# Kernel optimization log

Measured on AMD Instinct MI355X. Metric: run time of the kernel, lower is better.

## Reference

```python
import jax, jax.numpy as jnp
import numpy as np

B, IN, H = 4096, 1024, 1024


def setup_inputs() -> dict:
    key = jax.random.key(0)
    ks = jax.random.split(key, 16)
    s = 1.0 / np.sqrt(IN)
    inp = {
        "x_t": jax.random.normal(ks[0], (B, IN), jnp.float32),
        "h_prev": jax.random.normal(ks[1], (B, H), jnp.float32),
        "c_prev": jax.random.normal(ks[2], (B, H), jnp.float32),
        "W_xi": jax.random.uniform(ks[3], (H, IN), jnp.float32, -s, s),
        "W_hi": jax.random.normal(ks[4], (H, H), jnp.float32) / np.sqrt(H),
        "b_i": jnp.zeros((H,), jnp.float32),
        "W_xf": jax.random.uniform(ks[5], (H, IN), jnp.float32, -s, s),
        "W_hf": jax.random.normal(ks[6], (H, H), jnp.float32) / np.sqrt(H),
        "b_f": jnp.ones((H,), jnp.float32),
        "W_xg": jax.random.uniform(ks[7], (H, IN), jnp.float32, -s, s),
        "W_hg": jax.random.normal(ks[8], (H, H), jnp.float32) / np.sqrt(H),
        "b_g": jnp.zeros((H,), jnp.float32),
        "W_xo": jax.random.uniform(ks[9], (H, IN), jnp.float32, -s, s),
        "W_ho": jax.random.normal(ks[10], (H, H), jnp.float32) / np.sqrt(H),
        "b_o": jnp.zeros((H,), jnp.float32),
    }
    return inp


def reference(x_t, h_prev, c_prev,
              W_xi, W_hi, b_i,
              W_xf, W_hf, b_f,
              W_xg, W_hg, b_g,
              W_xo, W_ho, b_o):
    # i/f/g/o gates: sigmoid/sigmoid/tanh/sigmoid of (x W_x^T + h W_h^T + b)
    i_t = jax.nn.sigmoid(x_t @ W_xi.T + h_prev @ W_hi.T + b_i)
    f_t = jax.nn.sigmoid(x_t @ W_xf.T + h_prev @ W_hf.T + b_f)
    g_t = jnp.tanh(x_t @ W_xg.T + h_prev @ W_hg.T + b_g)
    o_t = jax.nn.sigmoid(x_t @ W_xo.T + h_prev @ W_ho.T + b_o)
    c_t = f_t * c_prev + i_t * g_t
    h_t = o_t * jnp.tanh(c_t)
    return (h_t, c_t)
```

## Files before the change

### kernel.cpp

```cpp
#include <hip/hip_runtime.h>
#include <hip/hip_bf16.h>


constexpr int Mdim = 4096;
constexpr int Ndim = 4096;
constexpr int Kdim = 2048;
constexpr int Hdim = 1024;
constexpr int BM = 256;
constexpr int BN = 256;
constexpr int BK = 32;
constexpr int NT = Kdim / BK;

using short8 = __attribute__((ext_vector_type(8))) short;
using f32x4  = __attribute__((ext_vector_type(4))) float;

__device__ __forceinline__ float sigmoid_(float x) {
    return 1.f / (1.f + __expf(-x));
}
__device__ __forceinline__ float tanh_(float x) {
    float e = __expf(2.f * x);
    return (e - 1.f) / (e + 1.f);
}

__global__ void build_A(const float* __restrict__ x, const float* __restrict__ h,
                        __hip_bfloat16* __restrict__ A) {
    int idx = blockIdx.x * 256 + threadIdx.x;
    int row = idx >> 8;
    int c8  = (idx & 255) * 8;
    const float* src = (c8 < 1024) ? (x + (size_t)row * 1024 + c8)
                                   : (h + (size_t)row * 1024 + (c8 - 1024));
    float4 f0 = ((const float4*)src)[0];
    float4 f1 = ((const float4*)src)[1];
    union { short8 v; __hip_bfloat16 e[8]; } u;
    u.e[0] = __float2bfloat16(f0.x); u.e[1] = __float2bfloat16(f0.y);
    u.e[2] = __float2bfloat16(f0.z); u.e[3] = __float2bfloat16(f0.w);
    u.e[4] = __float2bfloat16(f1.x); u.e[5] = __float2bfloat16(f1.y);
    u.e[6] = __float2bfloat16(f1.z); u.e[7] = __float2bfloat16(f1.w);
    *(short8*)(A + (size_t)row * Kdim + c8) = u.v;
}

__global__ void build_B(const float* __restrict__ Wxi, const float* __restrict__ Whi,
                        const float* __restrict__ Wxf, const float* __restrict__ Whf,
                        const float* __restrict__ Wxg, const float* __restrict__ Whg,
                        const float* __restrict__ Wxo, const float* __restrict__ Who,
                        __hip_bfloat16* __restrict__ B) {
    int idx = blockIdx.x * 256 + threadIdx.x;
    int n  = idx >> 8;
    int c8 = (idx & 255) * 8;
    int g = (n >> 4) & 3;
    int j = ((n >> 6) << 4) | (n & 15);
    const float* Wx = (g == 0) ? Wxi : (g == 1) ? Wxf : (g == 2) ? Wxg : Wxo;
    const float* Wh = (g == 0) ? Whi : (g == 1) ? Whf : (g == 2) ? Whg : Who;
    const float* src = (c8 < 1024) ? (Wx + (size_t)j * 1024 + c8)
                                   : (Wh + (size_t)j * 1024 + (c8 - 1024));
    float4 f0 = ((const float4*)src)[0];
    float4 f1 = ((const float4*)src)[1];
    union { short8 v; __hip_bfloat16 e[8]; } u;
    u.e[0] = __float2bfloat16(f0.x); u.e[1] = __float2bfloat16(f0.y);
    u.e[2] = __float2bfloat16(f0.z); u.e[3] = __float2bfloat16(f0.w);
    u.e[4] = __float2bfloat16(f1.x); u.e[5] = __float2bfloat16(f1.y);
    u.e[6] = __float2bfloat16(f1.z); u.e[7] = __float2bfloat16(f1.w);
    *(short8*)(B + (size_t)n * Kdim + c8) = u.v;
}

__launch_bounds__(512, 1)
__global__ void lstm_gemm(const __hip_bfloat16* __restrict__ A,
                          const __hip_bfloat16* __restrict__ B,
                          const float* __restrict__ c_prev,
                          const float* __restrict__ b_i, const float* __restrict__ b_f,
                          const float* __restrict__ b_g, const float* __restrict__ b_o,
                          float* __restrict__ out_h, float* __restrict__ out_c) {
    __shared__ __hip_bfloat16 lds[4][2][BM * BK];

    const int tid  = threadIdx.x;
    const int lane = tid & 63;
    const int w    = tid >> 6;
    const int wr   = w >> 2;
    const int wc   = w & 3;
    const int l15  = lane & 15, lhi = lane >> 4;

    int bid = blockIdx.x;
    int swz = (bid & 7) * 32 + (bid >> 3);
    const int bm = (swz >> 4) * BM;
    const int bn = (swz & 15) * BN;

    const int srow  = tid >> 2;
    const int scole = (((tid & 3) * 16) ^ (((tid >> 2) & 6) << 3)) >> 1;

    const int koff = (lhi * 16) ^ ((l15 & 6) << 3);

#define STAGE(s, kt)                                                            \
    do {                                                                        \
        _Pragma("unroll")                                                       \
        for (int i_ = 0; i_ < 2; ++i_)                                          \
            __builtin_amdgcn_global_load_lds(                                   \
                (const __attribute__((address_space(1))) unsigned*)(            \
                    A + (size_t)(bm + i_ * 128 + srow) * Kdim + (kt) + scole),  \
                (__attribute__((address_space(3))) unsigned*)(                  \
                    (char*)&lds[s][0][0] + i_ * 8192 + tid * 16), 16, 0, 0);    \
        _Pragma("unroll")                                                       \
        for (int i_ = 0; i_ < 2; ++i_)                                          \
            __builtin_amdgcn_global_load_lds(                                   \
                (const __attribute__((address_space(1))) unsigned*)(            \
                    B + (size_t)(bn + i_ * 128 + srow) * Kdim + (kt) + scole),  \
                (__attribute__((address_space(3))) unsigned*)(                  \
                    (char*)&lds[s][1][0] + i_ * 8192 + tid * 16), 16, 0, 0);    \
    } while (0)

    f32x4 acc[8][4];
#pragma unroll
    for (int a = 0; a < 8; ++a)
#pragma unroll
        for (int b = 0; b < 4; ++b)
            acc[a][b] = (f32x4){0.f, 0.f, 0.f, 0.f};

    STAGE(0, 0);
    STAGE(1, BK);
    STAGE(2, 2 * BK);
    asm volatile("s_waitcnt vmcnt(8)" ::: "memory");
    __builtin_amdgcn_s_barrier();
    __builtin_amdgcn_sched_barrier(0);

    for (int t = 0; t < NT; ++t) {
        if (t + 3 < NT) STAGE((t + 3) & 3, (t + 3) * BK);

        const char* As = (const char*)&lds[t & 3][0][0];
        const char* Bs = (const char*)&lds[t & 3][1][0];

        short8 bfr[4];
#pragma unroll
        for (int b = 0; b < 4; ++b)
            bfr[b] = *(const short8*)(Bs + (wc * 64 + b * 16 + l15) * 64 + koff);

        __builtin_amdgcn_s_setprio(1);
#pragma unroll
        for (int a = 0; a < 8; ++a) {
            short8 af = *(const short8*)(As + (wr * 128 + a * 16 + l15) * 64 + koff);
#pragma unroll
            for (int b = 0; b < 4; ++b)
                acc[a][b] = __builtin_amdgcn_mfma_f32_16x16x32_bf16(af, bfr[b], acc[a][b], 0, 0, 0);
        }
        __builtin_amdgcn_s_setprio(0);

        if (t < NT - 3)       asm volatile("s_waitcnt vmcnt(8)" ::: "memory");
        else if (t == NT - 3) asm volatile("s_waitcnt vmcnt(4)" ::: "memory");
        else if (t == NT - 2) asm volatile("s_waitcnt vmcnt(0)" ::: "memory");
        if (t < NT - 1) {
            __builtin_amdgcn_s_barrier();
            __builtin_amdgcn_sched_barrier(0);
        }
    }
#undef STAGE

    const int j0 = ((bn + wc * 64) >> 6) * 16 + l15;
    const float bi  = b_i[j0];
    const float bf_ = b_f[j0];
    const float bg  = b_g[j0];
    const float bo  = b_o[j0];

#pragma unroll
    for (int a = 0; a < 8; ++a) {
        int mbase = bm + wr * 128 + a * 16 + lhi * 4;
#pragma unroll
        for (int r = 0; r < 4; ++r) {
            int m = mbase + r;
            float vi = acc[a][0][r] + bi;
            float vf = acc[a][1][r] + bf_;
            float vg = acc[a][2][r] + bg;
            float vo = acc[a][3][r] + bo;
            float it = sigmoid_(vi);
            float ft = sigmoid_(vf);
            float gt = tanh_(vg);
            float ot = sigmoid_(vo);
            float cp = c_prev[(size_t)m * Hdim + j0];
            float ct = ft * cp + it * gt;
            float ht = ot * tanh_(ct);
            out_h[(size_t)m * Hdim + j0] = ht;
            out_c[(size_t)m * Hdim + j0] = ct;
        }
    }
}

extern "C" void kernel_launch(void* const* d_in, const int* in_sizes, int n_in,
                              void* d_out, int out_size, void* d_ws, size_t ws_size,
                              hipStream_t stream) {
    const float* x_t    = (const float*)d_in[0];
    const float* h_prev = (const float*)d_in[1];
    const float* c_prev = (const float*)d_in[2];
    const float* W_xi   = (const float*)d_in[3];
    const float* W_hi   = (const float*)d_in[4];
    const float* b_i    = (const float*)d_in[5];
    const float* W_xf   = (const float*)d_in[6];
    const float* W_hf   = (const float*)d_in[7];
    const float* b_f    = (const float*)d_in[8];
    const float* W_xg   = (const float*)d_in[9];
    const float* W_hg   = (const float*)d_in[10];
    const float* b_g    = (const float*)d_in[11];
    const float* W_xo   = (const float*)d_in[12];
    const float* W_ho   = (const float*)d_in[13];
    const float* b_o    = (const float*)d_in[14];

    float* out_h = (float*)d_out;
    float* out_c = out_h + (size_t)Mdim * Hdim;

    __hip_bfloat16* Abf = (__hip_bfloat16*)d_ws;
    __hip_bfloat16* Bbf = Abf + (size_t)Mdim * Kdim;

    build_A<<<4096, 256, 0, stream>>>(x_t, h_prev, Abf);
    build_B<<<4096, 256, 0, stream>>>(W_xi, W_hi, W_xf, W_hf, W_xg, W_hg, W_xo, W_ho, Bbf);

    lstm_gemm<<<dim3((Mdim / BM) * (Ndim / BN)), 512, 0, stream>>>(
        Abf, Bbf, c_prev, b_i, b_f, b_g, b_o, out_h, out_c);
}
```

Measured before the change: 91.31 us.

## Restructure GEMM main loop into 8-wave ping-pong schedule with BK=64 sub-stages

Replaces the 4-stage single-phase K loop with a double-buffered BK=64 loop split into four half-tile MFMA clusters separated by barriers. Global-to-LDS loads for upcoming sub-tiles are interleaved between the clusters, and LDS fragment reads are spread across them. The goal is to overlap memory traffic with MFMA work more finely and reduce loop overhead. In exchange it adds more barriers per iteration and tighter vmcnt accounting, which could stall waves or race if the counts are wrong.

```diff
diff --git a/kernel.cpp b/kernel.cpp
--- a/kernel.cpp
+++ b/kernel.cpp
@@ -8,7 +8,7 @@
 constexpr int Hdim = 1024;
 constexpr int BM = 256;
 constexpr int BN = 256;
-constexpr int BK = 32;
+constexpr int BK = 64;
 constexpr int NT = Kdim / BK;
 
 using short8 = __attribute__((ext_vector_type(8))) short;
@@ -63,6 +63,13 @@
     *(short8*)(B + (size_t)n * Kdim + c8) = u.v;
 }
 
+#define BAR()                                    \
+    do {                                         \
+        asm volatile("" ::: "memory");           \
+        __builtin_amdgcn_s_barrier();            \
+        __builtin_amdgcn_sched_barrier(0);       \
+    } while (0)
+
 __launch_bounds__(512, 1)
 __global__ void lstm_gemm(const __hip_bfloat16* __restrict__ A,
                           const __hip_bfloat16* __restrict__ B,
@@ -70,7 +77,7 @@
                           const float* __restrict__ b_i, const float* __restrict__ b_f,
                           const float* __restrict__ b_g, const float* __restrict__ b_o,
                           float* __restrict__ out_h, float* __restrict__ out_c) {
-    __shared__ __hip_bfloat16 lds[4][2][BM * BK];
+    __shared__ __hip_bfloat16 lds[2][2][2][256 * 32];
 
     const int tid  = threadIdx.x;
     const int lane = tid & 63;
@@ -89,23 +96,22 @@
 
     const int koff = (lhi * 16) ^ ((l15 & 6) << 3);
 
-#define STAGE(s, kt)                                                            \
+#define STG(dstbase, srcptr, growbase, kcol)                                    \
     do {                                                                        \
         _Pragma("unroll")                                                       \
         for (int i_ = 0; i_ < 2; ++i_)                                          \
             __builtin_amdgcn_global_load_lds(                                   \
                 (const __attribute__((address_space(1))) unsigned*)(            \
-                    A + (size_t)(bm + i_ * 128 + srow) * Kdim + (kt) + scole),  \
+                    (srcptr) + (size_t)((growbase) + i_ * 128 + srow) * Kdim    \
+                    + (kcol) + scole),                                          \
                 (__attribute__((address_space(3))) unsigned*)(                  \
-                    (char*)&lds[s][0][0] + i_ * 8192 + tid * 16), 16, 0, 0);    \
-        _Pragma("unroll")                                                       \
-        for (int i_ = 0; i_ < 2; ++i_)                                          \
-            __builtin_amdgcn_global_load_lds(                                   \
-                (const __attribute__((address_space(1))) unsigned*)(            \
-                    B + (size_t)(bn + i_ * 128 + srow) * Kdim + (kt) + scole),  \
-                (__attribute__((address_space(3))) unsigned*)(                  \
-                    (char*)&lds[s][1][0] + i_ * 8192 + tid * 16), 16, 0, 0);    \
+                    (char*)(dstbase) + i_ * 8192 + tid * 16), 16, 0, 0);        \
     } while (0)
+
+#define RDA(d, kk, a) (*(const short8*)((const char*)&lds[d][0][kk][0] + \
+                        (wr * 128 + (a) * 16 + l15) * 64 + koff))
+#define RDB(d, kk, b) (*(const short8*)((const char*)&lds[d][1][kk][0] + \
+                        (wc * 64 + (b) * 16 + l15) * 64 + koff))
 
     f32x4 acc[8][4];
 #pragma unroll
@@ -114,43 +120,89 @@
         for (int b = 0; b < 4; ++b)
             acc[a][b] = (f32x4){0.f, 0.f, 0.f, 0.f};
 
-    STAGE(0, 0);
-    STAGE(1, BK);
-    STAGE(2, 2 * BK);
-    asm volatile("s_waitcnt vmcnt(8)" ::: "memory");
-    __builtin_amdgcn_s_barrier();
-    __builtin_amdgcn_sched_barrier(0);
+    STG(&lds[0][0][0][0], A, bm, 0);
+    STG(&lds[0][1][0][0], B, bn, 0);
+    STG(&lds[0][0][1][0], A, bm, 32);
+    STG(&lds[0][1][1][0], B, bn, 32);
+    STG(&lds[1][0][0][0], A, bm, 64);
+    STG(&lds[1][1][0][0], B, bn, 64);
+    asm volatile("s_waitcnt vmcnt(4)" ::: "memory");
+    BAR();
 
     for (int t = 0; t < NT; ++t) {
-        if (t + 3 < NT) STAGE((t + 3) & 3, (t + 3) * BK);
-
-        const char* As = (const char*)&lds[t & 3][0][0];
-        const char* Bs = (const char*)&lds[t & 3][1][0];
-
-        short8 bfr[4];
-#pragma unroll
-        for (int b = 0; b < 4; ++b)
-            bfr[b] = *(const short8*)(Bs + (wc * 64 + b * 16 + l15) * 64 + koff);
-
-        __builtin_amdgcn_s_setprio(1);
-#pragma unroll
-        for (int a = 0; a < 8; ++a) {
-            short8 af = *(const short8*)(As + (wr * 128 + a * 16 + l15) * 64 + koff);
-#pragma unroll
-            for (int b = 0; b < 4; ++b)
-                acc[a][b] = __builtin_amdgcn_mfma_f32_16x16x32_bf16(af, bfr[b], acc[a][b], 0, 0, 0);
-        }
-        __builtin_amdgcn_s_setprio(0);
-
-        if (t < NT - 3)       asm volatile("s_waitcnt vmcnt(8)" ::: "memory");
-        else if (t == NT - 3) asm volatile("s_waitcnt vmcnt(4)" ::: "memory");
+        const int d = t & 1;
+
+        short8 af0 = RDA(d, 0, 0), af1 = RDA(d, 0, 1), af2 = RDA(d, 0, 2), af3 = RDA(d, 0, 3);
+        short8 bf0[4];
+#pragma unroll
+        for (int b = 0; b < 4; ++b) bf0[b] = RDB(d, 0, b);
+        if (t + 1 < NT) {
+            STG(&lds[d ^ 1][0][1][0], A, bm, (t + 1) * BK + 32);
+            STG(&lds[d ^ 1][1][1][0], B, bn, (t + 1) * BK + 32);
+        }
+        BAR();
+        __builtin_amdgcn_s_setprio(1);
+#pragma unroll
+        for (int b = 0; b < 4; ++b) {
+            acc[0][b] = __builtin_amdgcn_mfma_f32_16x16x32_bf16(af0, bf0[b], acc[0][b], 0, 0, 0);
+            acc[1][b] = __builtin_amdgcn_mfma_f32_16x16x32_bf16(af1, bf0[b], acc[1][b], 0, 0, 0);
+            acc[2][b] = __builtin_amdgcn_mfma_f32_16x16x32_bf16(af2, bf0[b], acc[2][b], 0, 0, 0);
+            acc[3][b] = __builtin_amdgcn_mfma_f32_16x16x32_bf16(af3, bf0[b], acc[3][b], 0, 0, 0);
+        }
+        __builtin_amdgcn_s_setprio(0);
+        BAR();
+
+        short8 af4 = RDA(d, 0, 4), af5 = RDA(d, 0, 5), af6 = RDA(d, 0, 6), af7 = RDA(d, 0, 7);
+        BAR();
+        __builtin_amdgcn_s_setprio(1);
+#pragma unroll
+        for (int b = 0; b < 4; ++b) {
+            acc[4][b] = __builtin_amdgcn_mfma_f32_16x16x32_bf16(af4, bf0[b], acc[4][b], 0, 0, 0);
+            acc[5][b] = __builtin_amdgcn_mfma_f32_16x16x32_bf16(af5, bf0[b], acc[5][b], 0, 0, 0);
+            acc[6][b] = __builtin_amdgcn_mfma_f32_16x16x32_bf16(af6, bf0[b], acc[6][b], 0, 0, 0);
+            acc[7][b] = __builtin_amdgcn_mfma_f32_16x16x32_bf16(af7, bf0[b], acc[7][b], 0, 0, 0);
+        }
+        __builtin_amdgcn_s_setprio(0);
+        BAR();
+
+        af0 = RDA(d, 1, 0); af1 = RDA(d, 1, 1); af2 = RDA(d, 1, 2); af3 = RDA(d, 1, 3);
+        short8 bf1[4];
+#pragma unroll
+        for (int b = 0; b < 4; ++b) bf1[b] = RDB(d, 1, b);
+        if (t + 2 < NT)
+            STG(&lds[d][0][0][0], A, bm, (t + 2) * BK);
+        BAR();
+        __builtin_amdgcn_s_setprio(1);
+#pragma unroll
+        for (int b = 0; b < 4; ++b) {
+            acc[0][b] = __builtin_amdgcn_mfma_f32_16x16x32_bf16(af0, bf1[b], acc[0][b], 0, 0, 0);
+            acc[1][b] = __builtin_amdgcn_mfma_f32_16x16x32_bf16(af1, bf1[b], acc[1][b], 0, 0, 0);
+            acc[2][b] = __builtin_amdgcn_mfma_f32_16x16x32_bf16(af2, bf1[b], acc[2][b], 0, 0, 0);
+            acc[3][b] = __builtin_amdgcn_mfma_f32_16x16x32_bf16(af3, bf1[b], acc[3][b], 0, 0, 0);
+        }
+        __builtin_amdgcn_s_setprio(0);
+        BAR();
+
+        af4 = RDA(d, 1, 4); af5 = RDA(d, 1, 5); af6 = RDA(d, 1, 6); af7 = RDA(d, 1, 7);
+        if (t + 2 < NT)
+            STG(&lds[d][1][0][0], B, bn, (t + 2) * BK);
+        BAR();
+        __builtin_amdgcn_s_setprio(1);
+#pragma unroll
+        for (int b = 0; b < 4; ++b) {
+            acc[4][b] = __builtin_amdgcn_mfma_f32_16x16x32_bf16(af4, bf1[b], acc[4][b], 0, 0, 0);
+            acc[5][b] = __builtin_amdgcn_mfma_f32_16x16x32_bf16(af5, bf1[b], acc[5][b], 0, 0, 0);
+            acc[6][b] = __builtin_amdgcn_mfma_f32_16x16x32_bf16(af6, bf1[b], acc[6][b], 0, 0, 0);
+            acc[7][b] = __builtin_amdgcn_mfma_f32_16x16x32_bf16(af7, bf1[b], acc[7][b], 0, 0, 0);
+        }
+        __builtin_amdgcn_s_setprio(0);
+        if (t < NT - 2)       asm volatile("s_waitcnt vmcnt(4)" ::: "memory");
         else if (t == NT - 2) asm volatile("s_waitcnt vmcnt(0)" ::: "memory");
-        if (t < NT - 1) {
-            __builtin_amdgcn_s_barrier();
-            __builtin_amdgcn_sched_barrier(0);
-        }
+        BAR();
     }
-#undef STAGE
+#undef STG
+#undef RDA
+#undef RDB
 
     const int j0 = ((bn + wc * 64) >> 6) * 16 + l15;
     const float bi  = b_i[j0];
```

After: 90.76 us. Within noise of the previous version (-0.6%).

## Double BK to 64 with two-stage LDS buffering and full-tile fragment preloading

Applied to the files above, without the earlier changes.

The K tile grows from 32 to 64, so the GEMM loop runs half as many iterations with two MFMA k-steps each, and the four-deep LDS ring becomes a two-stage double buffer. All A and B fragments for a tile are loaded into registers before the MFMA burst, and the LDS swizzle changes to fit 128-byte rows. Each iteration now drains all outstanding loads before its barrier, so the prefetch distance is one tile instead of three. That may expose global-load latency that the deeper pipeline used to hide, and the larger register fragments raise register pressure.

```diff
diff --git a/kernel.cpp b/kernel.cpp
--- a/kernel.cpp
+++ b/kernel.cpp
@@ -8,7 +8,7 @@
 constexpr int Hdim = 1024;
 constexpr int BM = 256;
 constexpr int BN = 256;
-constexpr int BK = 32;
+constexpr int BK = 64;
 constexpr int NT = Kdim / BK;
 
 using short8 = __attribute__((ext_vector_type(8))) short;
@@ -63,6 +63,8 @@
     *(short8*)(B + (size_t)n * Kdim + c8) = u.v;
 }
 
+#define RD(p) (*(const short8*)(p))
+
 __launch_bounds__(512, 1)
 __global__ void lstm_gemm(const __hip_bfloat16* __restrict__ A,
                           const __hip_bfloat16* __restrict__ B,
@@ -70,7 +72,7 @@
                           const float* __restrict__ b_i, const float* __restrict__ b_f,
                           const float* __restrict__ b_g, const float* __restrict__ b_o,
                           float* __restrict__ out_h, float* __restrict__ out_c) {
-    __shared__ __hip_bfloat16 lds[4][2][BM * BK];
+    __shared__ __hip_bfloat16 lds[2][2][2][128 * 64];
 
     const int tid  = threadIdx.x;
     const int lane = tid & 63;
@@ -84,27 +86,30 @@
     const int bm = (swz >> 4) * BM;
     const int bn = (swz & 15) * BN;
 
-    const int srow  = tid >> 2;
-    const int scole = (((tid & 3) * 16) ^ (((tid >> 2) & 6) << 3)) >> 1;
-
-    const int koff = (lhi * 16) ^ ((l15 & 6) << 3);
-
-#define STAGE(s, kt)                                                            \
+    const int srow_  = tid >> 3;
+    const int schunk = ((tid & 7) ^ ((tid >> 3) & 7)) * 8;
+
+    const int swz4 = (l15 & 7) << 4;
+    const int kof0 = (lhi * 16) ^ swz4;
+    const int kof1 = (64 + lhi * 16) ^ swz4;
+
+#define STG1(dstbase, byteoff, srcptr, grow, kcol)                              \
+    __builtin_amdgcn_global_load_lds(                                           \
+        (const __attribute__((address_space(1))) unsigned*)(                    \
+            (srcptr) + (size_t)((grow) + srow_) * Kdim + (kcol) + schunk),      \
+        (__attribute__((address_space(3))) unsigned*)(                          \
+            (char*)(dstbase) + (byteoff) + tid * 16), 16, 0, 0)
+
+#define STAGE_TILE(s, kc)                                                       \
     do {                                                                        \
-        _Pragma("unroll")                                                       \
-        for (int i_ = 0; i_ < 2; ++i_)                                          \
-            __builtin_amdgcn_global_load_lds(                                   \
-                (const __attribute__((address_space(1))) unsigned*)(            \
-                    A + (size_t)(bm + i_ * 128 + srow) * Kdim + (kt) + scole),  \
-                (__attribute__((address_space(3))) unsigned*)(                  \
-                    (char*)&lds[s][0][0] + i_ * 8192 + tid * 16), 16, 0, 0);    \
-        _Pragma("unroll")                                                       \
-        for (int i_ = 0; i_ < 2; ++i_)                                          \
-            __builtin_amdgcn_global_load_lds(                                   \
-                (const __attribute__((address_space(1))) unsigned*)(            \
-                    B + (size_t)(bn + i_ * 128 + srow) * Kdim + (kt) + scole),  \
-                (__attribute__((address_space(3))) unsigned*)(                  \
-                    (char*)&lds[s][1][0] + i_ * 8192 + tid * 16), 16, 0, 0);    \
+        STG1(&lds[s][1][0][0], 0,    B, bn + 0,   kc);                          \
+        STG1(&lds[s][1][0][0], 8192, B, bn + 64,  kc);                          \
+        STG1(&lds[s][1][1][0], 0,    B, bn + 128, kc);                          \
+        STG1(&lds[s][1][1][0], 8192, B, bn + 192, kc);                          \
+        STG1(&lds[s][0][0][0], 0,    A, bm + 0,   kc);                          \
+        STG1(&lds[s][0][0][0], 8192, A, bm + 64,  kc);                          \
+        STG1(&lds[s][0][1][0], 0,    A, bm + 128, kc);                          \
+        STG1(&lds[s][0][1][0], 8192, A, bm + 192, kc);                          \
     } while (0)
 
     f32x4 acc[8][4];
@@ -114,43 +119,50 @@
         for (int b = 0; b < 4; ++b)
             acc[a][b] = (f32x4){0.f, 0.f, 0.f, 0.f};
 
-    STAGE(0, 0);
-    STAGE(1, BK);
-    STAGE(2, 2 * BK);
-    asm volatile("s_waitcnt vmcnt(8)" ::: "memory");
+    STAGE_TILE(0, 0);
+    __builtin_amdgcn_sched_barrier(0);
+    asm volatile("s_waitcnt vmcnt(0)" ::: "memory");
     __builtin_amdgcn_s_barrier();
-    __builtin_amdgcn_sched_barrier(0);
 
     for (int t = 0; t < NT; ++t) {
-        if (t + 3 < NT) STAGE((t + 3) & 3, (t + 3) * BK);
-
-        const char* As = (const char*)&lds[t & 3][0][0];
-        const char* Bs = (const char*)&lds[t & 3][1][0];
-
-        short8 bfr[4];
-#pragma unroll
-        for (int b = 0; b < 4; ++b)
-            bfr[b] = *(const short8*)(Bs + (wc * 64 + b * 16 + l15) * 64 + koff);
+        const int d = t & 1;
+
+        if (t + 1 < NT) STAGE_TILE(d ^ 1, (t + 1) * BK);
+
+        const char* Ab = (const char*)&lds[d][0][wr][0] + l15 * 128;
+        const char* Bb = (const char*)&lds[d][1][wc >> 1][0] + ((wc & 1) * 64 + l15) * 128;
+
+        short8 af[8][2], bf[4][2];
+#pragma unroll
+        for (int a = 0; a < 8; ++a) {
+            af[a][0] = RD(Ab + a * 2048 + kof0);
+            af[a][1] = RD(Ab + a * 2048 + kof1);
+        }
+#pragma unroll
+        for (int b = 0; b < 4; ++b) {
+            bf[b][0] = RD(Bb + b * 2048 + kof0);
+            bf[b][1] = RD(Bb + b * 2048 + kof1);
+        }
 
         __builtin_amdgcn_s_setprio(1);
 #pragma unroll
-        for (int a = 0; a < 8; ++a) {
-            short8 af = *(const short8*)(As + (wr * 128 + a * 16 + l15) * 64 + koff);
+        for (int a = 0; a < 8; ++a)
 #pragma unroll
             for (int b = 0; b < 4; ++b)
-                acc[a][b] = __builtin_amdgcn_mfma_f32_16x16x32_bf16(af, bfr[b], acc[a][b], 0, 0, 0);
-        }
+#pragma unroll
+                for (int kk = 0; kk < 2; ++kk)
+                    acc[a][b] = __builtin_amdgcn_mfma_f32_16x16x32_bf16(
+                        af[a][kk], bf[b][kk], acc[a][b], 0, 0, 0);
         __builtin_amdgcn_s_setprio(0);
 
-        if (t < NT - 3)       asm volatile("s_waitcnt vmcnt(8)" ::: "memory");
-        else if (t == NT - 3) asm volatile("s_waitcnt vmcnt(4)" ::: "memory");
-        else if (t == NT - 2) asm volatile("s_waitcnt vmcnt(0)" ::: "memory");
-        if (t < NT - 1) {
+        if (t + 1 < NT) {
+            __builtin_amdgcn_sched_barrier(0);
+            asm volatile("s_waitcnt vmcnt(0) lgkmcnt(0)" ::: "memory");
             __builtin_amdgcn_s_barrier();
-            __builtin_amdgcn_sched_barrier(0);
         }
     }
-#undef STAGE
+#undef STG1
+#undef STAGE_TILE
 
     const int j0 = ((bn + wc * 64) >> 6) * 16 + l15;
     const float bi  = b_i[j0];
```

After: 86.34 us. -5.5%, faster.
